# Performance work log

Measured on AMD Instinct MI355X. Metric: run time of the kernel, lower is better.

## Reference

```python
import jax, jax.numpy as jnp
import numpy as np

EPSILON = 1e-8
NUM_STEPS = 1000
S_OFFSET = 0.0001
POWER = 2
CLIPMAX = 0.999
B = 1048576


def _schedule():
    t = jnp.arange(0, NUM_STEPS + 1, dtype=jnp.float32)
    f_t = jnp.cos(np.pi / 2 * (t / NUM_STEPS + S_OFFSET) / (1 + S_OFFSET)) ** POWER
    alpha_bars = f_t / f_t[0]
    betas = jnp.concatenate([jnp.zeros([1], jnp.float32), 1.0 - alpha_bars[1:] / alpha_bars[:-1]])
    betas = jnp.minimum(betas, CLIPMAX)
    sigmas = jnp.sqrt(betas[1:] * ((1.0 - alpha_bars[:-1]) / (1.0 - alpha_bars[1:])))
    sigmas = jnp.concatenate([jnp.zeros([1], jnp.float32), sigmas])
    return alpha_bars, betas, sigmas


def setup_inputs() -> dict:
    key = jax.random.key(0)
    k1, k2, k3, k4, k5 = jax.random.split(key, 5)
    lt = jax.random.normal(k1, (B, 6), dtype=jnp.float32)
    predicted_l0 = jax.random.normal(k2, (B, 6), dtype=jnp.float32)
    pred_lattice = jax.random.normal(k3, (B, 3, 3), dtype=jnp.float32)
    z_noise = jax.random.normal(k4, (B, 6), dtype=jnp.float32)  # torch.randn_like(lt), frozen
    t = jax.random.randint(k5, (B,), 0, NUM_STEPS, dtype=jnp.int64)
    alpha_bars, betas, sigmas = _schedule()
    return {
        "lt": lt,
        "predicted_l0": predicted_l0,
        "pred_lattice": pred_lattice,
        "alpha_bars": alpha_bars,
        "betas": betas,
        "sigmas": sigmas,
        "z_noise": z_noise,
        "t": t,
    }


def reference(lt, predicted_l0, pred_lattice, alpha_bars, betas, sigmas, z_noise, t):
    # VP_lattice.reverse
    alpha = 1.0 - betas[t]
    alpha = jnp.maximum(alpha, 1.0 - betas[-2])  # clamp_min
    alpha_bar = alpha_bars[t]
    sigma = sigmas[t][:, None]

    # polar_decomposition: only the symmetric factor L_tilda = V diag(S) V^T is used
    _, S, Vt = jnp.linalg.svd(pred_lattice, full_matrices=False)  # (B,3),(B,3,3)
    L = jnp.einsum("bji,bj,bjk->bik", Vt, S, Vt)  # Vt^T @ diag(S) @ Vt
    L = (L + jnp.swapaxes(L, 1, 2)) / 2  # symmetrize

    # symmetric_matrix_to_vector: upper triangular incl. diagonal
    vec = jnp.stack([L[:, 0, 0], L[:, 0, 1], L[:, 0, 2], L[:, 1, 1], L[:, 1, 2], L[:, 2, 2]], axis=1)

    predicted_noise = lt - (vec + predicted_l0) / 2
    z = jnp.where((t > 1)[:, None], z_noise, jnp.zeros_like(z_noise))
    coef = (1.0 / jnp.sqrt(alpha + EPSILON))[:, None]
    scale = ((1.0 - alpha) / jnp.sqrt(1.0 - alpha_bar + EPSILON))[:, None]
    return coef * (lt - scale * predicted_noise) + sigma * z
```

## Files before the change

### kernel.cpp

```cpp
#include <hip/hip_runtime.h>
#include <stdint.h>


#define NUM_STEPS 1000
#define TBL 1008
#define BLOCK 256
#define WAVES 4
#define RPB 256

#define W_PLAT 0
#define W_LT   576
#define W_PL0  960
#define W_ZN   1344
#define W_T    1728
#define W_SZF  1792
#define W_SZB  7168

#define AS1 __attribute__((address_space(1)))
#define AS3 __attribute__((address_space(3)))

typedef float v2f __attribute__((ext_vector_type(2)));

__device__ __forceinline__ void dma16nt(const void* g, void* s) {
    __builtin_amdgcn_global_load_lds((const AS1 void*)g, (AS3 void*)s, 16, 0, 2);
}

__global__ __launch_bounds__(256) void sched_kernel(
    const float* __restrict__ alpha_bars,
    const float* __restrict__ betas,
    const float* __restrict__ sigmas,
    float4* __restrict__ ws)
{
    int j = blockIdx.x * blockDim.x + threadIdx.x;
    if (j >= TBL) return;
    float4 v = make_float4(0.f, 0.f, 0.f, 0.f);
    if (j <= NUM_STEPS) {
        float beta_last = betas[NUM_STEPS - 1];
        float alpha = 1.0f - fminf(betas[j], beta_last);
        float coef  = 1.0f / sqrtf(alpha + 1e-8f);
        float scale = (1.0f - alpha) / sqrtf(1.0f - alpha_bars[j] + 1e-8f);
        v.x = coef * (1.0f - scale);
        v.y = 0.5f * coef * scale;
        v.z = (j > 1) ? sigmas[j] : 0.0f;
    }
    ws[j] = v;
}

__device__ __forceinline__ void sqrtm_vec(const float* pr, float vv[6])
{
    float a00 = pr[0], a01 = pr[1], a02 = pr[2];
    float a10 = pr[3], a11 = pr[4], a12 = pr[5];
    float a20 = pr[6], a21 = pr[7], a22 = pr[8];

    float m00 = a00*a00 + a10*a10 + a20*a20;
    float m01 = a00*a01 + a10*a11 + a20*a21;
    float m02 = a00*a02 + a10*a12 + a20*a22;
    float m11 = a01*a01 + a11*a11 + a21*a21;
    float m12 = a01*a02 + a11*a12 + a21*a22;
    float m22 = a02*a02 + a12*a12 + a22*a22;

    float q  = (m00 + m11 + m22) * (1.0f/3.0f);
    float b00 = m00 - q, b11 = m11 - q, b22 = m22 - q;
    float p1 = m01*m01 + m02*m02 + m12*m12;
    float p2 = b00*b00 + b11*b11 + b22*b22 + 2.0f*p1;
    float p  = sqrtf(p2 * (1.0f/6.0f));
    float detB = b00*(b11*b22 - m12*m12)
               - m01*(m01*b22 - m12*m02)
               + m02*(m01*m12 - b11*m02);
    float pinv = __fdividef(1.0f, fmaxf(p, 1e-20f));
    float r = 0.5f * detB * pinv * pinv * pinv;
    r = fminf(fmaxf(r, -1.0f), 1.0f);

    float ar = fabsf(r);
    float sq = sqrtf(1.0f - ar);
    float pl = 1.5707288f + ar * (-0.2121144f + ar * (0.0742610f - ar * 0.0187293f));
    float ac = sq * pl;
    float acr = (r >= 0.0f) ? ac : (3.14159265358979f - ac);
    float phi = acr * (1.0f/3.0f);
    float mu1 = q + 2.0f*p*__cosf(phi);
    float mu3 = q + 2.0f*p*__cosf(phi + 2.0943951023931953f);
    float mu2 = 3.0f*q - mu1 - mu3;
    float l1 = sqrtf(fmaxf(mu1, 0.0f));
    float l2 = sqrtf(fmaxf(mu2, 0.0f));
    float l3 = sqrtf(fmaxf(mu3, 0.0f));

    float IU   = l1 + l2 + l3;
    float IIU  = l1*(l2 + l3) + l2*l3;
    float IIIU = l1*l2*l3;
    float denom = (l1 + l2) * (l1 + l3) * (l2 + l3);
    float dinv  = __fdividef(1.0f, fmaxf(denom, 1e-25f));
    float sd = (IU*IU - IIU) * dinv;
    float td = IU * IIIU * dinv;
    float nd = -dinv;

    float mm00 = m00*m00 + m01*m01 + m02*m02;
    float mm01 = m00*m01 + m01*m11 + m02*m12;
    float mm02 = m00*m02 + m01*m12 + m02*m22;
    float mm11 = m01*m01 + m11*m11 + m12*m12;
    float mm12 = m01*m02 + m11*m12 + m12*m22;
    float mm22 = m02*m02 + m12*m12 + m22*m22;

    vv[0] = nd*mm00 + sd*m00 + td;
    vv[1] = nd*mm01 + sd*m01;
    vv[2] = nd*mm02 + sd*m02;
    vv[3] = nd*mm11 + sd*m11 + td;
    vv[4] = nd*mm12 + sd*m12;
    vv[5] = nd*mm22 + sd*m22 + td;
}

__global__ __launch_bounds__(BLOCK) void vp_lattice_kernel(
    const float* __restrict__ lt,
    const float* __restrict__ pl0,
    const float* __restrict__ plat,
    const float* __restrict__ alpha_bars,
    const float* __restrict__ betas,
    const float* __restrict__ sigmas,
    const float* __restrict__ z_noise,
    const int*   __restrict__ t,
    float* __restrict__ out,
    int n,
    const float4* __restrict__ coefs,
    int use_ws)
{
    __shared__ __align__(16) float sW[WAVES * W_SZF];

    const int tid  = threadIdx.x;
    const int lane = tid & 63;
    const int wv   = tid >> 6;
    const int rowW = blockIdx.x * RPB + wv * 64;

    float* w = sW + wv * W_SZF;

    if (rowW + 64 <= n) {
        const char* pP = (const char*)(plat    + (size_t)rowW * 9);
        const char* pL = (const char*)(lt      + (size_t)rowW * 6);
        const char* pQ = (const char*)(pl0     + (size_t)rowW * 6);
        const char* pZ = (const char*)(z_noise + (size_t)rowW * 6);
        const char* pT = (const char*)(t + rowW);
        char* wb = (char*)w;
        const int lb = lane * 16;

        dma16nt(pP + lb,        wb       );
        dma16nt(pP + 1024 + lb, wb + 1024);
        { int s = 2048 + lb;
          dma16nt((s < 2304) ? pP + s : pL + (s - 2304), wb + 2048); }
        { int s = 3072 + lb;
          dma16nt((s < 3840) ? pL + (s - 2304) : pQ + (s - 3840), wb + 3072); }
        dma16nt(pQ + 256 + lb,  wb + 4096);
        { int s = 5120 + lb;
          dma16nt((s < 5376) ? pQ + (s - 3840) : pZ + (s - 5376), wb + 5120); }
        { int s = 6144 + lb;
          dma16nt((s < 6912) ? pZ + (s - 5376) : pT + (s - 6912), wb + 6144); }

        asm volatile("s_waitcnt vmcnt(0)" ::: "memory");
        __builtin_amdgcn_sched_barrier(0);

        int ti = reinterpret_cast<const int*>(w + W_T)[lane];
        float4 cf;
        if (use_ws) {
            cf = coefs[ti];
        } else {
            float beta_last = betas[NUM_STEPS - 1];
            float alpha = 1.0f - fminf(betas[ti], beta_last);
            float coef  = 1.0f / sqrtf(alpha + 1e-8f);
            float scale = (1.0f - alpha) / sqrtf(1.0f - alpha_bars[ti] + 1e-8f);
            cf.x = coef * (1.0f - scale);
            cf.y = 0.5f * coef * scale;
            cf.z = (ti > 1) ? sigmas[ti] : 0.0f;
        }

        float va[6];
        sqrtm_vec(w + W_PLAT + lane * 9, va);

        const float* lr = w + W_LT  + lane * 6;
        const float* qr = w + W_PL0 + lane * 6;
        const float* zr = w + W_ZN  + lane * 6;

        float o[6];
#pragma unroll
        for (int c = 0; c < 6; ++c) {
            float lc = lr[c];
            o[c] = cf.x * lc + cf.y * (va[c] + qr[c]) + cf.z * zr[c];
        }

        v2f* oG = (v2f*)(out + (size_t)(rowW + lane) * 6);
        v2f s0; s0.x = o[0]; s0.y = o[1];
        v2f s1; s1.x = o[2]; s1.y = o[3];
        v2f s2; s2.x = o[4]; s2.y = o[5];
        __builtin_nontemporal_store(s0, oG + 0);
        __builtin_nontemporal_store(s1, oG + 1);
        __builtin_nontemporal_store(s2, oG + 2);
    } else {
        int row = rowW + lane;
        if (row >= n) return;
        float ab[9];
#pragma unroll
        for (int k = 0; k < 9; ++k) ab[k] = plat[(size_t)row * 9 + k];
        float va[6];
        sqrtm_vec(ab, va);
        int ti = t[row];
        float4 cf;
        if (use_ws) {
            cf = coefs[ti];
        } else {
            float beta_last = betas[NUM_STEPS - 1];
            float alpha = 1.0f - fminf(betas[ti], beta_last);
            float coef  = 1.0f / sqrtf(alpha + 1e-8f);
            float scale = (1.0f - alpha) / sqrtf(1.0f - alpha_bars[ti] + 1e-8f);
            cf.x = coef * (1.0f - scale);
            cf.y = 0.5f * coef * scale;
            cf.z = (ti > 1) ? sigmas[ti] : 0.0f;
        }
        size_t b6 = (size_t)row * 6;
#pragma unroll
        for (int c = 0; c < 6; ++c) {
            float lc = lt[b6 + c];
            out[b6 + c] = cf.x * lc + cf.y * (va[c] + pl0[b6 + c]) + cf.z * z_noise[b6 + c];
        }
    }
}

extern "C" void kernel_launch(void* const* d_in, const int* in_sizes, int n_in,
                              void* d_out, int out_size, void* d_ws, size_t ws_size,
                              hipStream_t stream) {
    const float* lt         = (const float*)d_in[0];
    const float* pl0        = (const float*)d_in[1];
    const float* plat       = (const float*)d_in[2];
    const float* alpha_bars = (const float*)d_in[3];
    const float* betas      = (const float*)d_in[4];
    const float* sigmas     = (const float*)d_in[5];
    const float* z_noise    = (const float*)d_in[6];
    const int*   t          = (const int*)d_in[7];
    float* out = (float*)d_out;
    float4* ws = (float4*)d_ws;

    int n = in_sizes[0] / 6;
    int use_ws = (ws != nullptr && ws_size >= (size_t)(TBL * sizeof(float4)));

    if (use_ws) {
        sched_kernel<<<(TBL + 255) / 256, 256, 0, stream>>>(alpha_bars, betas, sigmas, ws);
    }
    int grid = (n + RPB - 1) / RPB;
    vp_lattice_kernel<<<grid, BLOCK, 0, stream>>>(
        lt, pl0, plat, alpha_bars, betas, sigmas, z_noise, t, out, n, ws, use_ws);
}
```

Before: 151.0 us.

## Use persistent grid with double-buffered LDS staging per wave

Replaces the one-chunk-per-wave launch with a fixed 512-block persistent grid. Each wave loops over 64-row chunks and prefetches the next chunk into a second LDS buffer while it computes the current one. The goal is to hide global-to-LDS DMA latency and cut block launch overhead. In exchange it doubles LDS per block, which can lower occupancy, and with fewer waves in flight there is less latency hiding from other waves.

```diff
diff --git a/kernel.cpp b/kernel.cpp
--- a/kernel.cpp
+++ b/kernel.cpp
@@ -6,7 +6,7 @@
 #define TBL 1008
 #define BLOCK 256
 #define WAVES 4
-#define RPB 256
+#define GRID 512
 
 #define W_PLAT 0
 #define W_LT   576
@@ -14,8 +14,6 @@
 #define W_ZN   1344
 #define W_T    1728
 #define W_SZF  1792
-#define W_SZB  7168
-
 #define AS1 __attribute__((address_space(1)))
 #define AS3 __attribute__((address_space(3)))
 
@@ -44,6 +42,31 @@
         v.z = (j > 1) ? sigmas[j] : 0.0f;
     }
     ws[j] = v;
+}
+
+__device__ __forceinline__ void stage_chunk(
+    const float* __restrict__ lt,  const float* __restrict__ pl0,
+    const float* __restrict__ plat, const float* __restrict__ z_noise,
+    const int* __restrict__ t, int rowW, int lane, float* w)
+{
+    const char* pP = (const char*)(plat    + (size_t)rowW * 9);
+    const char* pL = (const char*)(lt      + (size_t)rowW * 6);
+    const char* pQ = (const char*)(pl0     + (size_t)rowW * 6);
+    const char* pZ = (const char*)(z_noise + (size_t)rowW * 6);
+    const char* pT = (const char*)(t + rowW);
+    char* wb = (char*)w;
+    const int lb = lane * 16;
+    dma16nt(pP + lb,        wb       );
+    dma16nt(pP + 1024 + lb, wb + 1024);
+    { int s = 2048 + lb;
+      dma16nt((s < 2304) ? pP + s : pL + (s - 2304), wb + 2048); }
+    { int s = 3072 + lb;
+      dma16nt((s < 3840) ? pL + (s - 2304) : pQ + (s - 3840), wb + 3072); }
+    dma16nt(pQ + 256 + lb,  wb + 4096);
+    { int s = 5120 + lb;
+      dma16nt((s < 5376) ? pQ + (s - 3840) : pZ + (s - 5376), wb + 5120); }
+    { int s = 6144 + lb;
+      dma16nt((s < 6912) ? pZ + (s - 5376) : pT + (s - 6912), wb + 6144); }
 }
 
 __device__ __forceinline__ void sqrtm_vec(const float* pr, float vv[6])
@@ -122,77 +145,75 @@
     const float4* __restrict__ coefs,
     int use_ws)
 {
-    __shared__ __align__(16) float sW[WAVES * W_SZF];
-
-    const int tid  = threadIdx.x;
-    const int lane = tid & 63;
-    const int wv   = tid >> 6;
-    const int rowW = blockIdx.x * RPB + wv * 64;
-
-    float* w = sW + wv * W_SZF;
-
-    if (rowW + 64 <= n) {
-        const char* pP = (const char*)(plat    + (size_t)rowW * 9);
-        const char* pL = (const char*)(lt      + (size_t)rowW * 6);
-        const char* pQ = (const char*)(pl0     + (size_t)rowW * 6);
-        const char* pZ = (const char*)(z_noise + (size_t)rowW * 6);
-        const char* pT = (const char*)(t + rowW);
-        char* wb = (char*)w;
-        const int lb = lane * 16;
-
-        dma16nt(pP + lb,        wb       );
-        dma16nt(pP + 1024 + lb, wb + 1024);
-        { int s = 2048 + lb;
-          dma16nt((s < 2304) ? pP + s : pL + (s - 2304), wb + 2048); }
-        { int s = 3072 + lb;
-          dma16nt((s < 3840) ? pL + (s - 2304) : pQ + (s - 3840), wb + 3072); }
-        dma16nt(pQ + 256 + lb,  wb + 4096);
-        { int s = 5120 + lb;
-          dma16nt((s < 5376) ? pQ + (s - 3840) : pZ + (s - 5376), wb + 5120); }
-        { int s = 6144 + lb;
-          dma16nt((s < 6912) ? pZ + (s - 5376) : pT + (s - 6912), wb + 6144); }
-
-        asm volatile("s_waitcnt vmcnt(0)" ::: "memory");
-        __builtin_amdgcn_sched_barrier(0);
-
-        int ti = reinterpret_cast<const int*>(w + W_T)[lane];
-        float4 cf;
-        if (use_ws) {
-            cf = coefs[ti];
-        } else {
-            float beta_last = betas[NUM_STEPS - 1];
-            float alpha = 1.0f - fminf(betas[ti], beta_last);
-            float coef  = 1.0f / sqrtf(alpha + 1e-8f);
-            float scale = (1.0f - alpha) / sqrtf(1.0f - alpha_bars[ti] + 1e-8f);
-            cf.x = coef * (1.0f - scale);
-            cf.y = 0.5f * coef * scale;
-            cf.z = (ti > 1) ? sigmas[ti] : 0.0f;
+    __shared__ __align__(16) float sW[WAVES * 2 * W_SZF];
+
+    const int lane = threadIdx.x & 63;
+    const int wv   = threadIdx.x >> 6;
+    const int wgid   = blockIdx.x * WAVES + wv;
+    const int totalW = gridDim.x * WAVES;
+    const int nchunks = n >> 6;
+
+    float* buf0 = sW + wv * 2 * W_SZF;
+    float* buf1 = buf0 + W_SZF;
+
+    if (wgid < nchunks) {
+        stage_chunk(lt, pl0, plat, z_noise, t, wgid * 64, lane, buf0);
+
+        int par = 0;
+        for (int c = wgid; c < nchunks; c += totalW) {
+            float* cur = par ? buf1 : buf0;
+            float* nxt = par ? buf0 : buf1;
+            par ^= 1;
+
+            asm volatile("s_waitcnt vmcnt(0)" ::: "memory");
+            __builtin_amdgcn_sched_barrier(0);
+
+            int ti = reinterpret_cast<const int*>(cur + W_T)[lane];
+            float4 cf;
+            if (use_ws) {
+                cf = coefs[ti];
+            } else {
+                float beta_last = betas[NUM_STEPS - 1];
+                float alpha = 1.0f - fminf(betas[ti], beta_last);
+                float coef  = 1.0f / sqrtf(alpha + 1e-8f);
+                float scale = (1.0f - alpha) / sqrtf(1.0f - alpha_bars[ti] + 1e-8f);
+                cf.x = coef * (1.0f - scale);
+                cf.y = 0.5f * coef * scale;
+                cf.z = (ti > 1) ? sigmas[ti] : 0.0f;
+            }
+            __builtin_amdgcn_sched_barrier(0);
+
+            int cn = c + totalW;
+            if (cn < nchunks)
+                stage_chunk(lt, pl0, plat, z_noise, t, cn * 64, lane, nxt);
+
+            const int rowW = c * 64;
+            float va[6];
+            sqrtm_vec(cur + W_PLAT + lane * 9, va);
+
+            const float* lr = cur + W_LT  + lane * 6;
+            const float* qr = cur + W_PL0 + lane * 6;
+            const float* zr = cur + W_ZN  + lane * 6;
+
+            float o[6];
+#pragma unroll
+            for (int k = 0; k < 6; ++k) {
+                float lc = lr[k];
+                o[k] = cf.x * lc + cf.y * (va[k] + qr[k]) + cf.z * zr[k];
+            }
+
+            v2f* oG = (v2f*)(out + (size_t)(rowW + lane) * 6);
+            v2f s0; s0.x = o[0]; s0.y = o[1];
+            v2f s1; s1.x = o[2]; s1.y = o[3];
+            v2f s2; s2.x = o[4]; s2.y = o[5];
+            __builtin_nontemporal_store(s0, oG + 0);
+            __builtin_nontemporal_store(s1, oG + 1);
+            __builtin_nontemporal_store(s2, oG + 2);
         }
-
-        float va[6];
-        sqrtm_vec(w + W_PLAT + lane * 9, va);
-
-        const float* lr = w + W_LT  + lane * 6;
-        const float* qr = w + W_PL0 + lane * 6;
-        const float* zr = w + W_ZN  + lane * 6;
-
-        float o[6];
-#pragma unroll
-        for (int c = 0; c < 6; ++c) {
-            float lc = lr[c];
-            o[c] = cf.x * lc + cf.y * (va[c] + qr[c]) + cf.z * zr[c];
-        }
-
-        v2f* oG = (v2f*)(out + (size_t)(rowW + lane) * 6);
-        v2f s0; s0.x = o[0]; s0.y = o[1];
-        v2f s1; s1.x = o[2]; s1.y = o[3];
-        v2f s2; s2.x = o[4]; s2.y = o[5];
-        __builtin_nontemporal_store(s0, oG + 0);
-        __builtin_nontemporal_store(s1, oG + 1);
-        __builtin_nontemporal_store(s2, oG + 2);
-    } else {
-        int row = rowW + lane;
-        if (row >= n) return;
+    }
+
+    for (int row = (nchunks << 6) + blockIdx.x * BLOCK + threadIdx.x;
+         row < n; row += gridDim.x * BLOCK) {
         float ab[9];
 #pragma unroll
         for (int k = 0; k < 9; ++k) ab[k] = plat[(size_t)row * 9 + k];
@@ -213,9 +234,9 @@
         }
         size_t b6 = (size_t)row * 6;
 #pragma unroll
-        for (int c = 0; c < 6; ++c) {
-            float lc = lt[b6 + c];
-            out[b6 + c] = cf.x * lc + cf.y * (va[c] + pl0[b6 + c]) + cf.z * z_noise[b6 + c];
+        for (int k = 0; k < 6; ++k) {
+            float lc = lt[b6 + k];
+            out[b6 + k] = cf.x * lc + cf.y * (va[k] + pl0[b6 + k]) + cf.z * z_noise[b6 + k];
         }
     }
 }
@@ -240,7 +261,6 @@
     if (use_ws) {
         sched_kernel<<<(TBL + 255) / 256, 256, 0, stream>>>(alpha_bars, betas, sigmas, ws);
     }
-    int grid = (n + RPB - 1) / RPB;
-    vp_lattice_kernel<<<grid, BLOCK, 0, stream>>>(
+    vp_lattice_kernel<<<GRID, BLOCK, 0, stream>>>(
         lt, pl0, plat, alpha_bars, betas, sigmas, z_noise, t, out, n, ws, use_ws);
 }
```

Measured after the change: 152.1 us. About the same (+0.7%).
